# Performance work log

Measured on AMD Instinct MI355X. Metric: run time of the kernel, lower is better.

## Reference

```python
import jax, jax.numpy as jnp
import numpy as np

N = 50000       # nodes per batched graph
E = 800000      # edges per batched graph
G = 256         # graphs per batch (for max-node pooling)
VOCAB = 120     # node types == embedding vocab
D_EMB = 32
D_H = 100
D_FC = 32
MIN_TYPE = 5    # min_type_count in compute_node_pair_mmd
CAP = 25        # max_nodes_per_type (deterministic: first CAP nodes per type)
KER_MUL = 2.0   # standard multi-kernel Gaussian MMD settings
KER_NUM = 5


def setup_inputs() -> dict:
    key = jax.random.key(0)
    ks = jax.random.split(key, 16)
    ri = lambda k, sh, hi: jax.random.randint(k, sh, 0, hi, dtype=jnp.int32)
    feat = ri(ks[0], (N,), VOCAB)
    feat_src = ri(ks[1], (N,), VOCAB)
    feat_tar = ri(ks[2], (N,), VOCAB)
    edge_index = ri(ks[3], (2, E), N)
    edge_index_src = ri(ks[4], (2, E), N)
    edge_index_tar = ri(ks[5], (2, E), N)
    graph_ids = (jnp.arange(N, dtype=jnp.int32) * G) // N  # sorted, even partition
    mask = (jax.random.uniform(ks[6], (N,)) > 0.1).astype(jnp.float32)
    embed = jax.random.normal(ks[7], (VOCAB, D_EMB)) * 0.02
    gcn_w = jax.random.normal(ks[8], (D_EMB, D_H)) * (1.0 / np.sqrt(D_EMB))
    gcn_b = jnp.zeros((D_H,), jnp.float32)
    fc_w = jax.random.normal(ks[9], (D_H, D_FC)) * (1.0 / np.sqrt(D_H))
    fc_b = jnp.zeros((D_FC,), jnp.float32)
    def_w = jax.random.normal(ks[10], (D_FC, 1)) * (1.0 / np.sqrt(D_FC))
    def_b = jnp.zeros((1,), jnp.float32)
    return dict(feat=feat, feat_src=feat_src, feat_tar=feat_tar,
                edge_index=edge_index, edge_index_src=edge_index_src,
                edge_index_tar=edge_index_tar, graph_ids=graph_ids, mask=mask,
                embed=embed, gcn_w=gcn_w, gcn_b=gcn_b, fc_w=fc_w, fc_b=fc_b,
                def_w=def_w, def_b=def_b)


def _graph_conv(x, ei, w, b):
    # DGL GraphConv, norm='both': D_out^{-1/2} A^T D_in^{-1/2} X W + b (degrees clamped to 1)
    src, dst = ei[0], ei[1]
    ones = jnp.ones((ei.shape[1],), x.dtype)
    outdeg = jnp.clip(jax.ops.segment_sum(ones, src, num_segments=N), 1.0)
    indeg = jnp.clip(jax.ops.segment_sum(ones, dst, num_segments=N), 1.0)
    h = (x @ w) * (outdeg ** -0.5)[:, None]          # [N, D_H], weight first (in<=out)
    agg = jax.ops.segment_sum(h[src], dst, num_segments=N)
    return agg * (indeg ** -0.5)[:, None] + b


def _mmd(src_types, tgt_types, src_feats, tgt_feats):
    # per-type multi-kernel Gaussian MMD; deterministic cap of CAP nodes/type
    def per_type(t):
        sm = (src_types == t)
        tm = (tgt_types == t)
        s_cnt = sm.sum()
        t_cnt = tm.sum()
        sv, si = jax.lax.top_k(sm.astype(jnp.float32), CAP)  # first CAP indices of type t
        tv, ti = jax.lax.top_k(tm.astype(jnp.float32), CAP)
        X = jnp.concatenate([src_feats[si], tgt_feats[ti]], 0)      # [2C, D]
        valid = jnp.concatenate([sv, tv]) > 0                        # [2C]
        pm = valid[:, None] & valid[None, :]
        D2 = jnp.sum((X[:, None, :] - X[None, :, :]) ** 2, -1)      # [2C, 2C]
        m = jnp.minimum(s_cnt, CAP).astype(jnp.float32)
        n = jnp.minimum(t_cnt, CAP).astype(jnp.float32)
        ntot = m + n
        bw = jnp.sum(jnp.where(pm, D2, 0.0)) / jnp.maximum(ntot * ntot - ntot, 1.0)
        bw = bw / (KER_MUL ** (KER_NUM // 2))
        bws = bw * (KER_MUL ** jnp.arange(KER_NUM, dtype=jnp.float32))
        K = jnp.sum(jnp.exp(-D2[None] / jnp.maximum(bws, 1e-8)[:, None, None]), 0)
        K = jnp.where(pm, K, 0.0)
        XX = K[:CAP, :CAP].sum() / jnp.maximum(m * m, 1.0)
        YY = K[CAP:, CAP:].sum() / jnp.maximum(n * n, 1.0)
        XY = K[:CAP, CAP:].sum() / jnp.maximum(m * n, 1.0)
        loss = XX + YY - 2.0 * XY
        inc = (s_cnt >= MIN_TYPE) & (t_cnt >= MIN_TYPE)
        return jnp.where(inc, loss, 0.0), inc.astype(jnp.float32)
    losses, incs = jax.vmap(per_type)(jnp.arange(1, VOCAB, dtype=jnp.int32))  # type 0 skipped
    cnt = incs.sum()
    return jnp.where(cnt > 0, losses.sum() / jnp.maximum(cnt, 1.0), 0.0)


def reference(feat, feat_src, feat_tar, edge_index, edge_index_src, edge_index_tar,
              graph_ids, mask, embed, gcn_w, gcn_b, fc_w, fc_b, def_w, def_b):
    def process(f, ei, msk):
        x = embed[f]
        if msk is not None:
            x = x * msk[:, None]
        h = jax.nn.relu(_graph_conv(x, ei, gcn_w, gcn_b))            # node feats 'h'
        pooled = jax.ops.segment_max(h, graph_ids, num_segments=G,
                                     indices_are_sorted=True)        # dgl.max_nodes
        return h, pooled

    _, pool = process(feat, edge_index, mask)
    h_src, pool_src = process(feat_src, edge_index_src, None)
    h_tar, pool_tar = process(feat_tar, edge_index_tar, None)

    x_batch_mmd = pool @ fc_w + fc_b        # [G, 32]
    x_src_mmd = pool_src @ fc_w + fc_b
    x_tar_mmd = pool_tar @ fc_w + fc_b
    src_node_feat = h_src @ fc_w + fc_b     # [N, 32]
    tgt_node_feat = h_tar @ fc_w + fc_b
    x_loss_mmd_node = _mmd(feat_src, feat_tar, src_node_feat, tgt_node_feat)
    defect_prob = jax.nn.sigmoid(x_batch_mmd @ def_w + def_b)  # [G, 1]
    # domain_clf output is not returned by the original forward, so it is skipped here.
    return (x_batch_mmd, defect_prob, x_src_mmd, x_tar_mmd, x_loss_mmd_node)
```

## Files before the change

kernel.cpp:

```cpp
#include <hip/hip_runtime.h>
#include <hip/hip_bf16.h>

#define Nn 50000
#define Ee 800000
#define Gg 256
#define VOC 120
#define DH 100
#define CAPc 25
#define NTYPE 119
#define NCHUNK 196
#define DR 4
#define DS 32
#define DWORDS 6250
#define NBIN 391
#define EBLK 782

__global__ void t_kernel(const float* __restrict__ embed, const float* __restrict__ gcn_w,
                         float* __restrict__ Tp) {
    int t = blockIdx.x;
    int j = threadIdx.x;
    if (j < DH) {
        float acc = 0.f;
#pragma unroll
        for (int k = 0; k < 32; ++k) acc = fmaf(embed[t * 32 + k], gcn_w[k * DH + j], acc);
        Tp[t * DH + j] = acc;
    }
}

__global__ void selcount_kernel(const int* __restrict__ feat_src, const int* __restrict__ feat_tar,
                                int* __restrict__ chunkcnt) {
    int chunk = blockIdx.x, side = blockIdx.y;
    const int* f = side ? feat_tar : feat_src;
    __shared__ int hist[VOC];
    int tid = threadIdx.x;
    if (tid < VOC) hist[tid] = 0;
    __syncthreads();
    int i = chunk * 256 + tid;
    if (i < Nn) atomicAdd(&hist[f[i]], 1);
    __syncthreads();
    if (tid < VOC) chunkcnt[(side * NCHUNK + chunk) * VOC + tid] = hist[tid];
}

__global__ __launch_bounds__(64) void selprefix_kernel(const int* __restrict__ chunkcnt,
                                                       int* __restrict__ base,
                                                       int* __restrict__ fullcnt) {
    int pair = blockIdx.x;
    int side = pair / VOC, t = pair - side * VOC;
    int lane = threadIdx.x;
    int run = 0;
    for (int c0 = 0; c0 < NCHUNK; c0 += 64) {
        int c = c0 + lane;
        int v = (c < NCHUNK) ? chunkcnt[(side * NCHUNK + c) * VOC + t] : 0;
        int inc = v;
#pragma unroll
        for (int o = 1; o < 64; o <<= 1) {
            int u = __shfl_up(inc, o, 64);
            if (lane >= o) inc += u;
        }
        if (c < NCHUNK) base[(side * NCHUNK + c) * VOC + t] = run + inc - v;
        run += __shfl(inc, 63, 64);
    }
    if (lane == 0) fullcnt[side * VOC + t] = run;
}

__global__ void selgather_kernel(const int* __restrict__ feat_src, const int* __restrict__ feat_tar,
                                 const int* __restrict__ base, int* __restrict__ selpos_src,
                                 int* __restrict__ selpos_tar) {
    int chunk = blockIdx.x, side = blockIdx.y;
    const int* f = side ? feat_tar : feat_src;
    int* selpos = side ? selpos_tar : selpos_src;
    __shared__ int types[256];
    int tid = threadIdx.x;
    int i = chunk * 256 + tid;
    int t = (i < Nn) ? f[i] : -1;
    types[tid] = t;
    int bv = 0;
    bool need = (t >= 1);
    if (need) {
        bv = base[(side * NCHUNK + chunk) * VOC + t];
        need = (bv < CAPc);
    }
    int any = __syncthreads_count((int)need);
    if (any == 0) return;
    if (need) {
        int rank = bv;
        for (int q = 0; q < 256; ++q)
            if (q < tid && types[q] == t) rank++;
        if (rank < CAPc) selpos[i] = (t - 1) * CAPc + rank;
    }
}

__global__ __launch_bounds__(256) void deghist_kernel(
        const int* __restrict__ ei0, const int* __restrict__ ei1, const int* __restrict__ ei2,
        int* __restrict__ partial) {
    int g = blockIdx.y;
    int r = blockIdx.x & (DR - 1), s = blockIdx.x >> 2;
    const int* ei = (g == 0) ? ei0 : (g == 1) ? ei1 : ei2;
    const uint4* a4 = (const uint4*)(ei + s * (Ee / DS));
    __shared__ int hist[DWORDS];
    int tid = threadIdx.x;
    for (int i = tid; i < DWORDS; i += 256) hist[i] = 0;
    __syncthreads();
    unsigned base = r * (2 * DWORDS);
    for (int idx = tid; idx < (Ee / DS) / 4; idx += 256) {
        uint4 v = a4[idx];
        unsigned q;
        q = v.x - base; if (q < 2 * DWORDS) atomicAdd(&hist[q >> 1], 1 << ((q & 1) * 16));
        q = v.y - base; if (q < 2 * DWORDS) atomicAdd(&hist[q >> 1], 1 << ((q & 1) * 16));
        q = v.z - base; if (q < 2 * DWORDS) atomicAdd(&hist[q >> 1], 1 << ((q & 1) * 16));
        q = v.w - base; if (q < 2 * DWORDS) atomicAdd(&hist[q >> 1], 1 << ((q & 1) * 16));
    }
    __syncthreads();
    int* outp = partial + ((size_t)(g * DR + r) * DS + s) * DWORDS;
    for (int i = tid; i < DWORDS; i += 256) outp[i] = hist[i];
}

__global__ __launch_bounds__(256) void degmerge_kernel(
        const int* __restrict__ partial,
        const int* __restrict__ feat0, const int* __restrict__ feat1, const int* __restrict__ feat2,
        const float* __restrict__ mask, float2* __restrict__ pc) {
    int idx = blockIdx.x * 256 + threadIdx.x;
    if (idx >= 3 * DR * DWORDS) return;
    int g = idx / (DR * DWORDS);
    int rem = idx - g * (DR * DWORDS);
    int r = rem / DWORDS, w = rem - r * DWORDS;
    const int* p = partial + ((size_t)(g * DR + r) * DS) * DWORDS + w;
    int sum = 0;
#pragma unroll 8
    for (int s = 0; s < DS; ++s) sum += p[s * DWORDS];
    int c0 = sum & 0xFFFF, c1 = sum >> 16;
    int n0 = r * (2 * DWORDS) + 2 * w;
    const int* ft = (g == 0) ? feat0 : (g == 1) ? feat1 : feat2;
    float cf0 = rsqrtf((float)max(c0, 1));
    float cf1 = rsqrtf((float)max(c1, 1));
    if (g == 0) {
        cf0 *= mask[n0];
        cf1 *= mask[n0 + 1];
    }
    float4 v = make_float4(cf0, __int_as_float(ft[n0]), cf1, __int_as_float(ft[n0 + 1]));
    ((float4*)(pc + (size_t)g * Nn))[r * DWORDS + w] = v;
}

__global__ __launch_bounds__(256) void bincount_kernel(const int* __restrict__ ei0,
                                                       const int* __restrict__ ei1,
                                                       const int* __restrict__ ei2,
                                                       int* __restrict__ cntbuf) {
    int g = blockIdx.y;
    const int* dst = ((g == 0) ? ei0 : (g == 1) ? ei1 : ei2) + Ee;
    __shared__ int cnt[NBIN];
    int tid = threadIdx.x;
    for (int i = tid; i < NBIN; i += 256) cnt[i] = 0;
    __syncthreads();
    int e0 = (blockIdx.x * 256 + tid) * 4;
    if (e0 < Ee) {
        uint4 d = *(const uint4*)&dst[e0];
        atomicAdd(&cnt[d.x >> 7], 1);
        atomicAdd(&cnt[d.y >> 7], 1);
        atomicAdd(&cnt[d.z >> 7], 1);
        atomicAdd(&cnt[d.w >> 7], 1);
    }
    __syncthreads();
    for (int i = tid; i < NBIN; i += 256)
        cntbuf[((size_t)g * NBIN + i) * EBLK + blockIdx.x] = cnt[i];
}

__global__ __launch_bounds__(64) void binprefix_kernel(const int* __restrict__ cntbuf,
                                                       int* __restrict__ ofsbuf,
                                                       int* __restrict__ bintot) {
    int pair = blockIdx.x;
    const int* src = cntbuf + (size_t)pair * EBLK;
    int* dst = ofsbuf + (size_t)pair * EBLK;
    int lane = threadIdx.x;
    int run = 0;
    for (int c0 = 0; c0 < EBLK; c0 += 64) {
        int c = c0 + lane;
        int v = (c < EBLK) ? src[c] : 0;
        int inc = v;
#pragma unroll
        for (int o = 1; o < 64; o <<= 1) {
            int u = __shfl_up(inc, o, 64);
            if (lane >= o) inc += u;
        }
        if (c < EBLK) dst[c] = run + inc - v;
        run += __shfl(inc, 63, 64);
    }
    if (lane == 0) bintot[pair] = run;
}

__global__ __launch_bounds__(64) void binbase_kernel(const int* __restrict__ bintot,
                                                     int* __restrict__ binbase) {
    int g = blockIdx.x;
    int lane = threadIdx.x;
    int run = 0;
    for (int c0 = 0; c0 < NBIN; c0 += 64) {
        int c = c0 + lane;
        int v = (c < NBIN) ? bintot[g * NBIN + c] : 0;
        int inc = v;
#pragma unroll
        for (int o = 1; o < 64; o <<= 1) {
            int u = __shfl_up(inc, o, 64);
            if (lane >= o) inc += u;
        }
        if (c < NBIN) binbase[g * NBIN + c] = run + inc - v;
        run += __shfl(inc, 63, 64);
    }
}

__global__ __launch_bounds__(256) void binscatter_kernel(const int* __restrict__ ei0,
                                                         const int* __restrict__ ei1,
                                                         const int* __restrict__ ei2,
                                                         const int* __restrict__ ofsbuf,
                                                         const int* __restrict__ binbase,
                                                         unsigned* __restrict__ ebuf) {
    int g = blockIdx.y;
    const int* ei = (g == 0) ? ei0 : (g == 1) ? ei1 : ei2;
    __shared__ int cur[NBIN];
    int tid = threadIdx.x;
    for (int i = tid; i < NBIN; i += 256)
        cur[i] = binbase[g * NBIN + i] + ofsbuf[((size_t)g * NBIN + i) * EBLK + blockIdx.x];
    __syncthreads();
    unsigned* eb = ebuf + (size_t)g * Ee;
    int e0 = (blockIdx.x * 256 + tid) * 4;
    if (e0 < Ee) {
        uint4 s = *(const uint4*)&ei[e0];
        uint4 d = *(const uint4*)&ei[Ee + e0];
        int p;
        p = atomicAdd(&cur[d.x >> 7], 1); eb[p] = ((d.x & 127u) << 16) | s.x;
        p = atomicAdd(&cur[d.y >> 7], 1); eb[p] = ((d.y & 127u) << 16) | s.y;
        p = atomicAdd(&cur[d.z >> 7], 1); eb[p] = ((d.z & 127u) << 16) | s.z;
        p = atomicAdd(&cur[d.w >> 7], 1); eb[p] = ((d.w & 127u) << 16) | s.w;
    }
}

__global__ __launch_bounds__(256, 2) void fused_wh_kernel(const unsigned* __restrict__ ebuf,
                                                          const float2* __restrict__ pc,
                                                          const int* __restrict__ binbase,
                                                          const int* __restrict__ bintot,
                                                          const float* __restrict__ Tp,
                                                          const int* __restrict__ selposall,
                                                          float* __restrict__ h_sel,
                                                          const float* __restrict__ gcn_b,
                                                          float* __restrict__ pool) {
    __shared__ float Wl[VOC * 128];
    __shared__ int cnt[128];
    int g = blockIdx.y, bin = blockIdx.x;
    int tid = threadIdx.x;

    float4* Wl4 = (float4*)Wl;
#pragma unroll
    for (int i = 0; i < 15; ++i) Wl4[tid + i * 256] = make_float4(0.f, 0.f, 0.f, 0.f);
    if (tid < 128) cnt[tid] = 0;
    __syncthreads();

    int base = binbase[g * NBIN + bin];
    int n = bintot[g * NBIN + bin];
    const unsigned* eb = ebuf + (size_t)g * Ee + base;
    const float2* pcg = pc + (size_t)g * Nn;
    for (int i = tid; i < n; i += 256) {
        unsigned e = eb[i];
        float2 p = pcg[e & 0xFFFFu];
        int dl = e >> 16;
        atomicAdd(&Wl[__float_as_int(p.y) * 128 + dl], p.x);
        atomicAdd(&cnt[dl], 1);
    }
    __syncthreads();

    int lane = tid & 63, wv = tid >> 6;
    int chcol = __builtin_amdgcn_readfirstlane(wv) * 25;
    const float* Tc = Tp + chcol;
    int r0 = bin * 128;
    int nr = min(128, Nn - r0);
    float accA[25], accB[25];
#pragma unroll
    for (int j = 0; j < 25; ++j) { accA[j] = 0.f; accB[j] = 0.f; }

    for (int t0 = 0; t0 < VOC; t0 += 8) {
        float wA8[8], wB8[8];
#pragma unroll
        for (int u = 0; u < 8; ++u) {
            wA8[u] = Wl[(t0 + u) * 128 + lane];
            wB8[u] = Wl[(t0 + u) * 128 + lane + 64];
        }
#pragma unroll
        for (int u = 0; u < 8; ++u) {
            const float* tr = Tc + (t0 + u) * DH;
#pragma unroll
            for (int j = 0; j < 25; ++j) {
                float tv = tr[j];
                accA[j] = fmaf(wA8[u], tv, accA[j]);
                accB[j] = fmaf(wB8[u], tv, accB[j]);
            }
        }
    }

    int rA = lane, rB = lane + 64;
    bool vA = rA < nr, vB = rB < nr;
    float rsA = vA ? rsqrtf((float)max(cnt[rA], 1)) : 0.f;
    float rsB = vB ? rsqrtf((float)max(cnt[rB], 1)) : 0.f;
    int growA = r0 + rA, growB = r0 + rB;
    int seg0 = (r0 * Gg) / Nn;
    int segA = (growA * Gg) / Nn, segB = (growB * Gg) / Nn;
    float bb[25];
#pragma unroll
    for (int j = 0; j < 25; ++j) bb[j] = gcn_b[wv * 25 + j];

    float v0[25], v1[25];
#pragma unroll
    for (int j = 0; j < 25; ++j) {
        float hA = vA ? fmaxf(fmaf(accA[j], rsA, bb[j]), 0.f) : 0.f;
        float hB = vB ? fmaxf(fmaf(accB[j], rsB, bb[j]), 0.f) : 0.f;
        accA[j] = hA;
        accB[j] = hB;
        v0[j] = fmaxf((vA && segA == seg0) ? hA : 0.f, (vB && segB == seg0) ? hB : 0.f);
        v1[j] = fmaxf((vA && segA != seg0) ? hA : 0.f, (vB && segB != seg0) ? hB : 0.f);
    }
#pragma unroll
    for (int m = 1; m < 64; m <<= 1) {
#pragma unroll
        for (int j = 0; j < 25; ++j) {
            v0[j] = fmaxf(v0[j], __shfl_xor(v0[j], m, 64));
            v1[j] = fmaxf(v1[j], __shfl_xor(v1[j], m, 64));
        }
    }
    if (lane == 0) {
        float* poolg = pool + g * (Gg * DH) + seg0 * DH + wv * 25;
        for (int j = 0; j < 25; ++j) atomicMax((int*)&poolg[j], __float_as_int(v0[j]));
        int segLast = ((r0 + nr - 1) * Gg) / Nn;
        if (segLast != seg0)
            for (int j = 0; j < 25; ++j) atomicMax((int*)&poolg[DH + j], __float_as_int(v1[j]));
    }

    if (g > 0) {
        const int* selpos = selposall + (size_t)(g - 1) * Nn;
        float* hs = h_sel + (size_t)(g == 2 ? NTYPE * CAPc * DH : 0);
        int spA = vA ? selpos[growA] : -1;
        int spB = vB ? selpos[growB] : -1;
        if (spA >= 0) {
            float* d = hs + (size_t)spA * DH + wv * 25;
            for (int j = 0; j < 25; ++j) d[j] = accA[j];
        }
        if (spB >= 0) {
            float* d = hs + (size_t)spB * DH + wv * 25;
            for (int j = 0; j < 25; ++j) d[j] = accB[j];
        }
    }
}

__global__ void poolgemm_kernel(const float* __restrict__ pool, const float* __restrict__ fc_w,
                                const float* __restrict__ fc_b, const float* __restrict__ def_w,
                                const float* __restrict__ def_b, float* __restrict__ out) {
    int g = blockIdx.x;
    __shared__ float xb[32];
    int tid = threadIdx.x;
    if (tid < 96) {
        int p = tid >> 5, j = tid & 31;
        float acc = fc_b[j];
        const float* pr = pool + p * (Gg * DH) + g * DH;
#pragma unroll 4
        for (int k = 0; k < DH; ++k) acc = fmaf(pr[k], fc_w[k * 32 + j], acc);
        int off = (p == 0) ? 0 : (p == 1 ? 8448 : 16640);
        out[off + g * 32 + j] = acc;
        if (p == 0) xb[j] = acc;
    }
    __syncthreads();
    if (tid < 32) {
        float v = xb[tid] * def_w[tid];
        for (int o = 16; o; o >>= 1) v += __shfl_down(v, o, 64);
        if (tid == 0) out[8192 + g] = 1.f / (1.f + expf(-(v + def_b[0])));
    }
}

__global__ __launch_bounds__(256) void xfeat_kernel(const float* __restrict__ h_sel,
                                                    const int* __restrict__ fullcnt,
                                                    const float* __restrict__ fc_w,
                                                    const float* __restrict__ fc_b,
                                                    float* __restrict__ X) {
    int t = blockIdx.x;
    __shared__ float fw[DH * 32];
    for (int i = threadIdx.x; i < DH * 32; i += 256) fw[i] = fc_w[i];
    __syncthreads();
    int cs = min(fullcnt[t + 1], CAPc);
    int ct = min(fullcnt[VOC + t + 1], CAPc);
    int j = threadIdx.x & 31, rg = threadIdx.x >> 5;
    for (int r = rg; r < 2 * CAPc; r += 8) {
        int side = r / CAPc, rr = r % CAPc;
        int cnt = side ? ct : cs;
        float acc = 0.f;
        if (rr < cnt) {
            const float* hr = h_sel + ((size_t)side * NTYPE * CAPc + (size_t)t * CAPc + rr) * DH;
            acc = fc_b[j];
#pragma unroll 4
            for (int k = 0; k < DH; ++k) acc = fmaf(hr[k], fw[k * 32 + j], acc);
        }
        X[(size_t)t * 1600 + r * 32 + j] = acc;
    }
}

__device__ __forceinline__ float block_reduce256(float v, float* red, int tid) {
    __syncthreads();
    red[tid] = v;
    __syncthreads();
    for (int s = 128; s > 0; s >>= 1) {
        if (tid < s) red[tid] += red[tid + s];
        __syncthreads();
    }
    return red[0];
}

__global__ __launch_bounds__(256) void mmd_kernel(const float* __restrict__ X,
                                                  const int* __restrict__ fullcnt,
                                                  float* __restrict__ losses) {
    int t = blockIdx.x;
    __shared__ float Xs[50 * 32];
    __shared__ float D2[50 * 50];
    __shared__ float red[256];
    int tid = threadIdx.x;
    for (int i = tid; i < 1600; i += 256) Xs[i] = X[(size_t)t * 1600 + i];
    __syncthreads();
    int scF = fullcnt[t + 1];
    int tcF = fullcnt[VOC + t + 1];
    int m = min(scF, CAPc), n2 = min(tcF, CAPc);
    float bwpart = 0.f;
    for (int idx = tid; idx < 2500; idx += 256) {
        int i = idx / 50, j = idx % 50;
        float d = 0.f;
#pragma unroll
        for (int k = 0; k < 32; ++k) {
            float df = Xs[i * 32 + k] - Xs[j * 32 + k];
            d = fmaf(df, df, d);
        }
        D2[idx] = d;
        bool vi = (i < CAPc) ? (i < m) : (i - CAPc < n2);
        bool vj = (j < CAPc) ? (j < m) : (j - CAPc < n2);
        if (vi && vj) bwpart += d;
    }
    float bwsum = block_reduce256(bwpart, red, tid);
    float ntot = (float)(m + n2);
    float bw = bwsum / fmaxf(ntot * ntot - ntot, 1.f) * 0.25f;
    float bws[5];
#pragma unroll
    for (int k = 0; k < 5; ++k) bws[k] = fmaxf(bw * (float)(1 << k), 1e-8f);
    float xx = 0.f, yy = 0.f, xy = 0.f;
    for (int idx = tid; idx < 2500; idx += 256) {
        int i = idx / 50, j = idx % 50;
        bool vi = (i < CAPc) ? (i < m) : (i - CAPc < n2);
        bool vj = (j < CAPc) ? (j < m) : (j - CAPc < n2);
        if (!(vi && vj)) continue;
        float d = D2[idx];
        float kv = 0.f;
#pragma unroll
        for (int k = 0; k < 5; ++k) kv += expf(-d / bws[k]);
        if (i < CAPc && j < CAPc) xx += kv;
        else if (i >= CAPc && j >= CAPc) yy += kv;
        else if (i < CAPc) xy += kv;
    }
    float rxx = block_reduce256(xx, red, tid);
    float ryy = block_reduce256(yy, red, tid);
    float rxy = block_reduce256(xy, red, tid);
    if (tid == 0) {
        float fm = (float)m, fn = (float)n2;
        float XX = rxx / fmaxf(fm * fm, 1.f);
        float YY = ryy / fmaxf(fn * fn, 1.f);
        float XY = rxy / fmaxf(fm * fn, 1.f);
        float loss = XX + YY - 2.f * XY;
        int inc = (scF >= 5 && tcF >= 5) ? 1 : 0;
        losses[t * 2 + 0] = inc ? loss : 0.f;
        losses[t * 2 + 1] = (float)inc;
    }
}

__global__ void final_kernel(const float* __restrict__ losses, float* __restrict__ out) {
    __shared__ float red[128], redc[128];
    int tid = threadIdx.x;
    float s = 0.f, c = 0.f;
    for (int t = tid; t < NTYPE; t += 128) {
        s += losses[t * 2];
        c += losses[t * 2 + 1];
    }
    red[tid] = s;
    redc[tid] = c;
    __syncthreads();
    for (int st = 64; st > 0; st >>= 1) {
        if (tid < st) {
            red[tid] += red[tid + st];
            redc[tid] += redc[tid + st];
        }
        __syncthreads();
    }
    if (tid == 0) out[24832] = redc[0] > 0.f ? red[0] / fmaxf(redc[0], 1.f) : 0.f;
}

extern "C" void kernel_launch(void* const* d_in, const int* in_sizes, int n_in,
                              void* d_out, int out_size, void* d_ws, size_t ws_size,
                              hipStream_t stream) {
    const int* feat = (const int*)d_in[0];
    const int* feat_src = (const int*)d_in[1];
    const int* feat_tar = (const int*)d_in[2];
    const int* ei0 = (const int*)d_in[3];
    const int* ei1 = (const int*)d_in[4];
    const int* ei2 = (const int*)d_in[5];
    const float* mask = (const float*)d_in[7];
    const float* embed = (const float*)d_in[8];
    const float* gcn_w = (const float*)d_in[9];
    const float* gcn_b = (const float*)d_in[10];
    const float* fc_w = (const float*)d_in[11];
    const float* fc_b = (const float*)d_in[12];
    const float* def_w = (const float*)d_in[13];
    const float* def_b = (const float*)d_in[14];
    float* out = (float*)d_out;

    char* wsb = (char*)d_ws;
    int* partial = (int*)(wsb + 0);
    float* Tp = (float*)(wsb + 9600000);
    float* pool = (float*)(wsb + 9660000);
    float2* pc = (float2*)(wsb + 9967200);
    int* selpos = (int*)(wsb + 11167200);
    float* h_sel = (float*)(wsb + 11567200);
    int* fullcnt = (int*)(wsb + 13947200);
    float* X = (float*)(wsb + 13948160);
    float* losses = (float*)(wsb + 14709760);
    int* chunkcnt = (int*)(wsb + 14710720);
    int* baseb = (int*)(wsb + 14898880);
    int* cntbuf = (int*)(wsb + 15087040);
    int* ofsbuf = (int*)(wsb + 18756200);
    int* bintot = (int*)(wsb + 22425400);
    int* binbase = (int*)(wsb + 22430400);
    unsigned* ebuf = (unsigned*)(wsb + 22435200);

    hipMemsetAsync(pool, 0, 3 * Gg * DH * sizeof(float), stream);
    hipMemsetAsync(selpos, 0xFF, 2 * Nn * sizeof(int), stream);

    t_kernel<<<VOC, 128, 0, stream>>>(embed, gcn_w, Tp);

    selcount_kernel<<<dim3(NCHUNK, 2), 256, 0, stream>>>(feat_src, feat_tar, chunkcnt);
    selprefix_kernel<<<2 * VOC, 64, 0, stream>>>(chunkcnt, baseb, fullcnt);
    selgather_kernel<<<dim3(NCHUNK, 2), 256, 0, stream>>>(feat_src, feat_tar, baseb,
                                                          selpos, selpos + Nn);

    bincount_kernel<<<dim3(EBLK, 3), 256, 0, stream>>>(ei0, ei1, ei2, cntbuf);
    binprefix_kernel<<<3 * NBIN, 64, 0, stream>>>(cntbuf, ofsbuf, bintot);
    binbase_kernel<<<3, 64, 0, stream>>>(bintot, binbase);
    binscatter_kernel<<<dim3(EBLK, 3), 256, 0, stream>>>(ei0, ei1, ei2, ofsbuf, binbase, ebuf);

    deghist_kernel<<<dim3(DR * DS, 3), 256, 0, stream>>>(ei0, ei1, ei2, partial);
    degmerge_kernel<<<(3 * DR * DWORDS + 255) / 256, 256, 0, stream>>>(partial, feat, feat_src,
                                                                       feat_tar, mask, pc);

    fused_wh_kernel<<<dim3(NBIN, 3), 256, 0, stream>>>(ebuf, pc, binbase, bintot, Tp, selpos,
                                                       h_sel, gcn_b, pool);

    poolgemm_kernel<<<Gg, 128, 0, stream>>>(pool, fc_w, fc_b, def_w, def_b, out);
    xfeat_kernel<<<NTYPE, 256, 0, stream>>>(h_sel, fullcnt, fc_w, fc_b, X);
    mmd_kernel<<<NTYPE, 256, 0, stream>>>(X, fullcnt, losses);
    final_kernel<<<1, 128, 0, stream>>>(losses, out);
}
```

Measured before the change: 250.1 us.

## Split per-bin type-weight LDS accumulation into two type-range passes

New measurement: 296.4 us. +18.5%, slower.

```diff
diff --git a/kernel.cpp b/kernel.cpp
--- a/kernel.cpp
+++ b/kernel.cpp
@@ -14,6 +14,7 @@
 #define DWORDS 6250
 #define NBIN 391
 #define EBLK 782
+#define TCH2 60
 
 __global__ void t_kernel(const float* __restrict__ embed, const float* __restrict__ gcn_w,
                          float* __restrict__ Tp) {
@@ -241,58 +242,82 @@
                                                           float* __restrict__ h_sel,
                                                           const float* __restrict__ gcn_b,
                                                           float* __restrict__ pool) {
-    __shared__ float Wl[VOC * 128];
+    __shared__ float Wl[TCH2 * 128];
     __shared__ int cnt[128];
     int g = blockIdx.y, bin = blockIdx.x;
     int tid = threadIdx.x;
-
-    float4* Wl4 = (float4*)Wl;
-#pragma unroll
-    for (int i = 0; i < 15; ++i) Wl4[tid + i * 256] = make_float4(0.f, 0.f, 0.f, 0.f);
     if (tid < 128) cnt[tid] = 0;
-    __syncthreads();
 
     int base = binbase[g * NBIN + bin];
     int n = bintot[g * NBIN + bin];
     const unsigned* eb = ebuf + (size_t)g * Ee + base;
     const float2* pcg = pc + (size_t)g * Nn;
-    for (int i = tid; i < n; i += 256) {
-        unsigned e = eb[i];
-        float2 p = pcg[e & 0xFFFFu];
-        int dl = e >> 16;
-        atomicAdd(&Wl[__float_as_int(p.y) * 128 + dl], p.x);
-        atomicAdd(&cnt[dl], 1);
-    }
-    __syncthreads();
 
     int lane = tid & 63, wv = tid >> 6;
-    int chcol = __builtin_amdgcn_readfirstlane(wv) * 25;
-    const float* Tc = Tp + chcol;
+    const float* Tc = Tp + wv * 25;
+    float accA[25], accB[25];
+#pragma unroll
+    for (int j = 0; j < 25; ++j) { accA[j] = 0.f; accB[j] = 0.f; }
+
+    float4* Wl4 = (float4*)Wl;
+    for (int pass = 0; pass < 2; ++pass) {
+        __syncthreads();
+#pragma unroll
+        for (int i = 0; i < 8; ++i) {
+            int idx = tid + i * 256;
+            if (idx < TCH2 * 32) Wl4[idx] = make_float4(0.f, 0.f, 0.f, 0.f);
+        }
+        __syncthreads();
+        int tlo = pass * TCH2;
+        for (int i = tid; i < n; i += 256) {
+            unsigned e = eb[i];
+            float2 p = pcg[e & 0xFFFFu];
+            int dl = e >> 16;
+            if (pass == 0) atomicAdd(&cnt[dl], 1);
+            unsigned tq = (unsigned)(__float_as_int(p.y) - tlo);
+            if (tq < TCH2) atomicAdd(&Wl[tq * 128 + dl], p.x);
+        }
+        __syncthreads();
+        const float* Tb = Tc + tlo * DH;
+        for (int t0 = 0; t0 < TCH2; t0 += 4) {
+            float w0A = Wl[(t0 + 0) * 128 + lane];
+            float w0B = Wl[(t0 + 0) * 128 + lane + 64];
+            float w1A = Wl[(t0 + 1) * 128 + lane];
+            float w1B = Wl[(t0 + 1) * 128 + lane + 64];
+            float w2A = Wl[(t0 + 2) * 128 + lane];
+            float w2B = Wl[(t0 + 2) * 128 + lane + 64];
+            float w3A = Wl[(t0 + 3) * 128 + lane];
+            float w3B = Wl[(t0 + 3) * 128 + lane + 64];
+            const float* tr = Tb + t0 * DH;
+#pragma unroll
+            for (int j = 0; j < 25; ++j) {
+                float tv = tr[j];
+                accA[j] = fmaf(w0A, tv, accA[j]);
+                accB[j] = fmaf(w0B, tv, accB[j]);
+            }
+#pragma unroll
+            for (int j = 0; j < 25; ++j) {
+                float tv = tr[DH + j];
+                accA[j] = fmaf(w1A, tv, accA[j]);
+                accB[j] = fmaf(w1B, tv, accB[j]);
+            }
+#pragma unroll
+            for (int j = 0; j < 25; ++j) {
+                float tv = tr[2 * DH + j];
+                accA[j] = fmaf(w2A, tv, accA[j]);
+                accB[j] = fmaf(w2B, tv, accB[j]);
+            }
+#pragma unroll
+            for (int j = 0; j < 25; ++j) {
+                float tv = tr[3 * DH + j];
+                accA[j] = fmaf(w3A, tv, accA[j]);
+                accB[j] = fmaf(w3B, tv, accB[j]);
+            }
+        }
+    }
+
     int r0 = bin * 128;
     int nr = min(128, Nn - r0);
-    float accA[25], accB[25];
-#pragma unroll
-    for (int j = 0; j < 25; ++j) { accA[j] = 0.f; accB[j] = 0.f; }
-
-    for (int t0 = 0; t0 < VOC; t0 += 8) {
-        float wA8[8], wB8[8];
-#pragma unroll
-        for (int u = 0; u < 8; ++u) {
-            wA8[u] = Wl[(t0 + u) * 128 + lane];
-            wB8[u] = Wl[(t0 + u) * 128 + lane + 64];
-        }
-#pragma unroll
-        for (int u = 0; u < 8; ++u) {
-            const float* tr = Tc + (t0 + u) * DH;
-#pragma unroll
-            for (int j = 0; j < 25; ++j) {
-                float tv = tr[j];
-                accA[j] = fmaf(wA8[u], tv, accA[j]);
-                accB[j] = fmaf(wB8[u], tv, accB[j]);
-            }
-        }
-    }
-
     int rA = lane, rB = lane + 64;
     bool vA = rA < nr, vB = rB < nr;
     float rsA = vA ? rsqrtf((float)max(cnt[rA], 1)) : 0.f;
```

## Merge independent stage kernels into block-dispatched launches to cut launch count

Applied to the files above, without the earlier changes.

New measurement: 215.0 us. -14.0%, faster.

```diff
diff --git a/kernel.cpp b/kernel.cpp
--- a/kernel.cpp
+++ b/kernel.cpp
@@ -15,176 +15,147 @@
 #define NBIN 391
 #define EBLK 782
 
-__global__ void t_kernel(const float* __restrict__ embed, const float* __restrict__ gcn_w,
-                         float* __restrict__ Tp) {
-    int t = blockIdx.x;
-    int j = threadIdx.x;
-    if (j < DH) {
-        float acc = 0.f;
-#pragma unroll
-        for (int k = 0; k < 32; ++k) acc = fmaf(embed[t * 32 + k], gcn_w[k * DH + j], acc);
-        Tp[t * DH + j] = acc;
-    }
-}
-
-__global__ void selcount_kernel(const int* __restrict__ feat_src, const int* __restrict__ feat_tar,
-                                int* __restrict__ chunkcnt) {
-    int chunk = blockIdx.x, side = blockIdx.y;
-    const int* f = side ? feat_tar : feat_src;
-    __shared__ int hist[VOC];
+#define P1_T 0
+#define P1_SEL 120
+#define P1_BIN 512
+#define P1_DEG 2858
+#define P1_PCLR 3242
+#define P1_SCLR 3317
+#define P1_TOT 3415
+#define P3_SELG 0
+#define P3_BSC 392
+#define P3_DMG 2738
+#define P3_TOT 3031
+
+__global__ __launch_bounds__(256) void prep_kernel(
+        const float* __restrict__ embed, const float* __restrict__ gcn_w, float* __restrict__ Tp,
+        const int* __restrict__ feat_src, const int* __restrict__ feat_tar,
+        int* __restrict__ chunkcnt,
+        const int* __restrict__ ei0, const int* __restrict__ ei1, const int* __restrict__ ei2,
+        int* __restrict__ cntbuf, int* __restrict__ partial,
+        float* __restrict__ pool, int* __restrict__ selpos) {
+    __shared__ int sm[DWORDS];
+    int bx = blockIdx.x;
     int tid = threadIdx.x;
-    if (tid < VOC) hist[tid] = 0;
-    __syncthreads();
-    int i = chunk * 256 + tid;
-    if (i < Nn) atomicAdd(&hist[f[i]], 1);
-    __syncthreads();
-    if (tid < VOC) chunkcnt[(side * NCHUNK + chunk) * VOC + tid] = hist[tid];
-}
-
-__global__ __launch_bounds__(64) void selprefix_kernel(const int* __restrict__ chunkcnt,
-                                                       int* __restrict__ base,
-                                                       int* __restrict__ fullcnt) {
-    int pair = blockIdx.x;
-    int side = pair / VOC, t = pair - side * VOC;
+
+    if (bx < P1_SEL) {
+        int t = bx - P1_T;
+        if (tid < DH) {
+            float acc = 0.f;
+#pragma unroll
+            for (int k = 0; k < 32; ++k) acc = fmaf(embed[t * 32 + k], gcn_w[k * DH + tid], acc);
+            Tp[t * DH + tid] = acc;
+        }
+        return;
+    }
+    if (bx < P1_BIN) {
+        int idx = bx - P1_SEL;
+        int side = idx / NCHUNK, chunk = idx - side * NCHUNK;
+        const int* f = side ? feat_tar : feat_src;
+        if (tid < VOC) sm[tid] = 0;
+        __syncthreads();
+        int i = chunk * 256 + tid;
+        if (i < Nn) atomicAdd(&sm[f[i]], 1);
+        __syncthreads();
+        if (tid < VOC) chunkcnt[(side * NCHUNK + chunk) * VOC + tid] = sm[tid];
+        return;
+    }
+    if (bx < P1_DEG) {
+        int idx = bx - P1_BIN;
+        int g = idx / EBLK, blk = idx - g * EBLK;
+        const int* dst = ((g == 0) ? ei0 : (g == 1) ? ei1 : ei2) + Ee;
+        for (int i = tid; i < NBIN; i += 256) sm[i] = 0;
+        __syncthreads();
+        int e0 = (blk * 256 + tid) * 4;
+        if (e0 < Ee) {
+            uint4 d = *(const uint4*)&dst[e0];
+            atomicAdd(&sm[d.x >> 7], 1);
+            atomicAdd(&sm[d.y >> 7], 1);
+            atomicAdd(&sm[d.z >> 7], 1);
+            atomicAdd(&sm[d.w >> 7], 1);
+        }
+        __syncthreads();
+        for (int i = tid; i < NBIN; i += 256)
+            cntbuf[((size_t)g * NBIN + i) * EBLK + blk] = sm[i];
+        return;
+    }
+    if (bx < P1_PCLR) {
+        int idx = bx - P1_DEG;
+        int g = idx / (DR * DS), rs = idx - g * (DR * DS);
+        int r = rs & (DR - 1), s = rs >> 2;
+        const int* ei = (g == 0) ? ei0 : (g == 1) ? ei1 : ei2;
+        const uint4* a4 = (const uint4*)(ei + s * (Ee / DS));
+        for (int i = tid; i < DWORDS; i += 256) sm[i] = 0;
+        __syncthreads();
+        unsigned base = r * (2 * DWORDS);
+        for (int idx2 = tid; idx2 < (Ee / DS) / 4; idx2 += 256) {
+            uint4 v = a4[idx2];
+            unsigned q;
+            q = v.x - base; if (q < 2 * DWORDS) atomicAdd(&sm[q >> 1], 1 << ((q & 1) * 16));
+            q = v.y - base; if (q < 2 * DWORDS) atomicAdd(&sm[q >> 1], 1 << ((q & 1) * 16));
+            q = v.z - base; if (q < 2 * DWORDS) atomicAdd(&sm[q >> 1], 1 << ((q & 1) * 16));
+            q = v.w - base; if (q < 2 * DWORDS) atomicAdd(&sm[q >> 1], 1 << ((q & 1) * 16));
+        }
+        __syncthreads();
+        int* outp = partial + ((size_t)(g * DR + r) * DS + s) * DWORDS;
+        for (int i = tid; i < DWORDS; i += 256) outp[i] = sm[i];
+        return;
+    }
+    if (bx < P1_SCLR) {
+        int i = (bx - P1_PCLR) * 256 + tid;
+        ((float4*)pool)[i] = make_float4(0.f, 0.f, 0.f, 0.f);
+        return;
+    }
+    {
+        int i = (bx - P1_SCLR) * 256 + tid;
+        if (i < 25000) ((int4*)selpos)[i] = make_int4(-1, -1, -1, -1);
+        return;
+    }
+}
+
+__global__ __launch_bounds__(64) void prefix_kernel(const int* __restrict__ chunkcnt,
+                                                    int* __restrict__ baseb,
+                                                    int* __restrict__ fullcnt,
+                                                    const int* __restrict__ cntbuf,
+                                                    int* __restrict__ ofsbuf,
+                                                    int* __restrict__ bintot) {
+    int bx = blockIdx.x;
     int lane = threadIdx.x;
-    int run = 0;
-    for (int c0 = 0; c0 < NCHUNK; c0 += 64) {
-        int c = c0 + lane;
-        int v = (c < NCHUNK) ? chunkcnt[(side * NCHUNK + c) * VOC + t] : 0;
-        int inc = v;
-#pragma unroll
-        for (int o = 1; o < 64; o <<= 1) {
-            int u = __shfl_up(inc, o, 64);
-            if (lane >= o) inc += u;
-        }
-        if (c < NCHUNK) base[(side * NCHUNK + c) * VOC + t] = run + inc - v;
-        run += __shfl(inc, 63, 64);
-    }
-    if (lane == 0) fullcnt[side * VOC + t] = run;
-}
-
-__global__ void selgather_kernel(const int* __restrict__ feat_src, const int* __restrict__ feat_tar,
-                                 const int* __restrict__ base, int* __restrict__ selpos_src,
-                                 int* __restrict__ selpos_tar) {
-    int chunk = blockIdx.x, side = blockIdx.y;
-    const int* f = side ? feat_tar : feat_src;
-    int* selpos = side ? selpos_tar : selpos_src;
-    __shared__ int types[256];
-    int tid = threadIdx.x;
-    int i = chunk * 256 + tid;
-    int t = (i < Nn) ? f[i] : -1;
-    types[tid] = t;
-    int bv = 0;
-    bool need = (t >= 1);
-    if (need) {
-        bv = base[(side * NCHUNK + chunk) * VOC + t];
-        need = (bv < CAPc);
-    }
-    int any = __syncthreads_count((int)need);
-    if (any == 0) return;
-    if (need) {
-        int rank = bv;
-        for (int q = 0; q < 256; ++q)
-            if (q < tid && types[q] == t) rank++;
-        if (rank < CAPc) selpos[i] = (t - 1) * CAPc + rank;
-    }
-}
-
-__global__ __launch_bounds__(256) void deghist_kernel(
-        const int* __restrict__ ei0, const int* __restrict__ ei1, const int* __restrict__ ei2,
-        int* __restrict__ partial) {
-    int g = blockIdx.y;
-    int r = blockIdx.x & (DR - 1), s = blockIdx.x >> 2;
-    const int* ei = (g == 0) ? ei0 : (g == 1) ? ei1 : ei2;
-    const uint4* a4 = (const uint4*)(ei + s * (Ee / DS));
-    __shared__ int hist[DWORDS];
-    int tid = threadIdx.x;
-    for (int i = tid; i < DWORDS; i += 256) hist[i] = 0;
-    __syncthreads();
-    unsigned base = r * (2 * DWORDS);
-    for (int idx = tid; idx < (Ee / DS) / 4; idx += 256) {
-        uint4 v = a4[idx];
-        unsigned q;
-        q = v.x - base; if (q < 2 * DWORDS) atomicAdd(&hist[q >> 1], 1 << ((q & 1) * 16));
-        q = v.y - base; if (q < 2 * DWORDS) atomicAdd(&hist[q >> 1], 1 << ((q & 1) * 16));
-        q = v.z - base; if (q < 2 * DWORDS) atomicAdd(&hist[q >> 1], 1 << ((q & 1) * 16));
-        q = v.w - base; if (q < 2 * DWORDS) atomicAdd(&hist[q >> 1], 1 << ((q & 1) * 16));
-    }
-    __syncthreads();
-    int* outp = partial + ((size_t)(g * DR + r) * DS + s) * DWORDS;
-    for (int i = tid; i < DWORDS; i += 256) outp[i] = hist[i];
-}
-
-__global__ __launch_bounds__(256) void degmerge_kernel(
-        const int* __restrict__ partial,
-        const int* __restrict__ feat0, const int* __restrict__ feat1, const int* __restrict__ feat2,
-        const float* __restrict__ mask, float2* __restrict__ pc) {
-    int idx = blockIdx.x * 256 + threadIdx.x;
-    if (idx >= 3 * DR * DWORDS) return;
-    int g = idx / (DR * DWORDS);
-    int rem = idx - g * (DR * DWORDS);
-    int r = rem / DWORDS, w = rem - r * DWORDS;
-    const int* p = partial + ((size_t)(g * DR + r) * DS) * DWORDS + w;
-    int sum = 0;
-#pragma unroll 8
-    for (int s = 0; s < DS; ++s) sum += p[s * DWORDS];
-    int c0 = sum & 0xFFFF, c1 = sum >> 16;
-    int n0 = r * (2 * DWORDS) + 2 * w;
-    const int* ft = (g == 0) ? feat0 : (g == 1) ? feat1 : feat2;
-    float cf0 = rsqrtf((float)max(c0, 1));
-    float cf1 = rsqrtf((float)max(c1, 1));
-    if (g == 0) {
-        cf0 *= mask[n0];
-        cf1 *= mask[n0 + 1];
-    }
-    float4 v = make_float4(cf0, __int_as_float(ft[n0]), cf1, __int_as_float(ft[n0 + 1]));
-    ((float4*)(pc + (size_t)g * Nn))[r * DWORDS + w] = v;
-}
-
-__global__ __launch_bounds__(256) void bincount_kernel(const int* __restrict__ ei0,
-                                                       const int* __restrict__ ei1,
-                                                       const int* __restrict__ ei2,
-                                                       int* __restrict__ cntbuf) {
-    int g = blockIdx.y;
-    const int* dst = ((g == 0) ? ei0 : (g == 1) ? ei1 : ei2) + Ee;
-    __shared__ int cnt[NBIN];
-    int tid = threadIdx.x;
-    for (int i = tid; i < NBIN; i += 256) cnt[i] = 0;
-    __syncthreads();
-    int e0 = (blockIdx.x * 256 + tid) * 4;
-    if (e0 < Ee) {
-        uint4 d = *(const uint4*)&dst[e0];
-        atomicAdd(&cnt[d.x >> 7], 1);
-        atomicAdd(&cnt[d.y >> 7], 1);
-        atomicAdd(&cnt[d.z >> 7], 1);
-        atomicAdd(&cnt[d.w >> 7], 1);
-    }
-    __syncthreads();
-    for (int i = tid; i < NBIN; i += 256)
-        cntbuf[((size_t)g * NBIN + i) * EBLK + blockIdx.x] = cnt[i];
-}
-
-__global__ __launch_bounds__(64) void binprefix_kernel(const int* __restrict__ cntbuf,
-                                                       int* __restrict__ ofsbuf,
-                                                       int* __restrict__ bintot) {
-    int pair = blockIdx.x;
-    const int* src = cntbuf + (size_t)pair * EBLK;
-    int* dst = ofsbuf + (size_t)pair * EBLK;
-    int lane = threadIdx.x;
-    int run = 0;
-    for (int c0 = 0; c0 < EBLK; c0 += 64) {
-        int c = c0 + lane;
-        int v = (c < EBLK) ? src[c] : 0;
-        int inc = v;
-#pragma unroll
-        for (int o = 1; o < 64; o <<= 1) {
-            int u = __shfl_up(inc, o, 64);
-            if (lane >= o) inc += u;
-        }
-        if (c < EBLK) dst[c] = run + inc - v;
-        run += __shfl(inc, 63, 64);
-    }
-    if (lane == 0) bintot[pair] = run;
+    if (bx < 2 * VOC) {
+        int side = bx / VOC, t = bx - side * VOC;
+        int run = 0;
+        for (int c0 = 0; c0 < NCHUNK; c0 += 64) {
+            int c = c0 + lane;
+            int v = (c < NCHUNK) ? chunkcnt[(side * NCHUNK + c) * VOC + t] : 0;
+            int inc = v;
+#pragma unroll
+            for (int o = 1; o < 64; o <<= 1) {
+                int u = __shfl_up(inc, o, 64);
+                if (lane >= o) inc += u;
+            }
+            if (c < NCHUNK) baseb[(side * NCHUNK + c) * VOC + t] = run + inc - v;
+            run += __shfl(inc, 63, 64);
+        }
+        if (lane == 0) fullcnt[side * VOC + t] = run;
+    } else {
+        int pair = bx - 2 * VOC;
+        const int* src = cntbuf + (size_t)pair * EBLK;
+        int* dst = ofsbuf + (size_t)pair * EBLK;
+        int run = 0;
+        for (int c0 = 0; c0 < EBLK; c0 += 64) {
+            int c = c0 + lane;
+            int v = (c < EBLK) ? src[c] : 0;
+            int inc = v;
+#pragma unroll
+            for (int o = 1; o < 64; o <<= 1) {
+                int u = __shfl_up(inc, o, 64);
+                if (lane >= o) inc += u;
+            }
+            if (c < EBLK) dst[c] = run + inc - v;
+            run += __shfl(inc, 63, 64);
+        }
+        if (lane == 0) bintot[pair] = run;
+    }
 }
 
 __global__ __launch_bounds__(64) void binbase_kernel(const int* __restrict__ bintot,
@@ -206,29 +177,84 @@
     }
 }
 
-__global__ __launch_bounds__(256) void binscatter_kernel(const int* __restrict__ ei0,
-                                                         const int* __restrict__ ei1,
-                                                         const int* __restrict__ ei2,
-                                                         const int* __restrict__ ofsbuf,
-                                                         const int* __restrict__ binbase,
-                                                         unsigned* __restrict__ ebuf) {
-    int g = blockIdx.y;
-    const int* ei = (g == 0) ? ei0 : (g == 1) ? ei1 : ei2;
-    __shared__ int cur[NBIN];
+__global__ __launch_bounds__(256) void scatter_kernel(
+        const int* __restrict__ feat_src, const int* __restrict__ feat_tar,
+        const int* __restrict__ baseb, int* __restrict__ selpos_src, int* __restrict__ selpos_tar,
+        const int* __restrict__ ei0, const int* __restrict__ ei1, const int* __restrict__ ei2,
+        const int* __restrict__ ofsbuf, const int* __restrict__ binbase,
+        unsigned* __restrict__ ebuf,
+        const int* __restrict__ partial, const int* __restrict__ feat0,
+        const float* __restrict__ mask, float2* __restrict__ pc) {
+    __shared__ int sm[NBIN];
+    int bx = blockIdx.x;
     int tid = threadIdx.x;
-    for (int i = tid; i < NBIN; i += 256)
-        cur[i] = binbase[g * NBIN + i] + ofsbuf[((size_t)g * NBIN + i) * EBLK + blockIdx.x];
-    __syncthreads();
-    unsigned* eb = ebuf + (size_t)g * Ee;
-    int e0 = (blockIdx.x * 256 + tid) * 4;
-    if (e0 < Ee) {
-        uint4 s = *(const uint4*)&ei[e0];
-        uint4 d = *(const uint4*)&ei[Ee + e0];
-        int p;
-        p = atomicAdd(&cur[d.x >> 7], 1); eb[p] = ((d.x & 127u) << 16) | s.x;
-        p = atomicAdd(&cur[d.y >> 7], 1); eb[p] = ((d.y & 127u) << 16) | s.y;
-        p = atomicAdd(&cur[d.z >> 7], 1); eb[p] = ((d.z & 127u) << 16) | s.z;
-        p = atomicAdd(&cur[d.w >> 7], 1); eb[p] = ((d.w & 127u) << 16) | s.w;
+
+    if (bx < P3_BSC) {
+        int idx = bx - P3_SELG;
+        int side = idx / NCHUNK, chunk = idx - side * NCHUNK;
+        const int* f = side ? feat_tar : feat_src;
+        int* selpos = side ? selpos_tar : selpos_src;
+        int i = chunk * 256 + tid;
+        int t = (i < Nn) ? f[i] : -1;
+        sm[tid] = t;
+        int bv = 0;
+        bool need = (t >= 1);
+        if (need) {
+            bv = baseb[(side * NCHUNK + chunk) * VOC + t];
+            need = (bv < CAPc);
+        }
+        int any = __syncthreads_count((int)need);
+        if (any == 0) return;
+        if (need) {
+            int rank = bv;
+            for (int q = 0; q < 256; ++q)
+                if (q < tid && sm[q] == t) rank++;
+            if (rank < CAPc) selpos[i] = (t - 1) * CAPc + rank;
+        }
+        return;
+    }
+    if (bx < P3_DMG) {
+        int idx = bx - P3_BSC;
+        int g = idx / EBLK, blk = idx - g * EBLK;
+        const int* ei = (g == 0) ? ei0 : (g == 1) ? ei1 : ei2;
+        for (int i = tid; i < NBIN; i += 256)
+            sm[i] = binbase[g * NBIN + i] + ofsbuf[((size_t)g * NBIN + i) * EBLK + blk];
+        __syncthreads();
+        unsigned* eb = ebuf + (size_t)g * Ee;
+        int e0 = (blk * 256 + tid) * 4;
+        if (e0 < Ee) {
+            uint4 s = *(const uint4*)&ei[e0];
+            uint4 d = *(const uint4*)&ei[Ee + e0];
+            int p;
+            p = atomicAdd(&sm[d.x >> 7], 1); eb[p] = ((d.x & 127u) << 16) | s.x;
+            p = atomicAdd(&sm[d.y >> 7], 1); eb[p] = ((d.y & 127u) << 16) | s.y;
+            p = atomicAdd(&sm[d.z >> 7], 1); eb[p] = ((d.z & 127u) << 16) | s.z;
+            p = atomicAdd(&sm[d.w >> 7], 1); eb[p] = ((d.w & 127u) << 16) | s.w;
+        }
+        return;
+    }
+    {
+        int idx = (bx - P3_DMG) * 256 + tid;
+        if (idx >= 3 * DR * DWORDS) return;
+        int g = idx / (DR * DWORDS);
+        int rem = idx - g * (DR * DWORDS);
+        int r = rem / DWORDS, w = rem - r * DWORDS;
+        const int* p = partial + ((size_t)(g * DR + r) * DS) * DWORDS + w;
+        int sum = 0;
+#pragma unroll 8
+        for (int s = 0; s < DS; ++s) sum += p[s * DWORDS];
+        int c0 = sum & 0xFFFF, c1 = sum >> 16;
+        int n0 = r * (2 * DWORDS) + 2 * w;
+        const int* ft = (g == 0) ? feat0 : (g == 1) ? feat_src : feat_tar;
+        float cf0 = rsqrtf((float)max(c0, 1));
+        float cf1 = rsqrtf((float)max(c1, 1));
+        if (g == 0) {
+            cf0 *= mask[n0];
+            cf1 *= mask[n0 + 1];
+        }
+        float4 v = make_float4(cf0, __int_as_float(ft[n0]), cf1, __int_as_float(ft[n0 + 1]));
+        ((float4*)(pc + (size_t)g * Nn))[r * DWORDS + w] = v;
+        return;
     }
 }
 
@@ -346,53 +372,58 @@
     }
 }
 
-__global__ void poolgemm_kernel(const float* __restrict__ pool, const float* __restrict__ fc_w,
-                                const float* __restrict__ fc_b, const float* __restrict__ def_w,
-                                const float* __restrict__ def_b, float* __restrict__ out) {
-    int g = blockIdx.x;
-    __shared__ float xb[32];
+__global__ __launch_bounds__(256) void post_kernel(const float* __restrict__ pool,
+                                                   const float* __restrict__ fc_w,
+                                                   const float* __restrict__ fc_b,
+                                                   const float* __restrict__ def_w,
+                                                   const float* __restrict__ def_b,
+                                                   float* __restrict__ out,
+                                                   const float* __restrict__ h_sel,
+                                                   const int* __restrict__ fullcnt,
+                                                   float* __restrict__ X) {
+    __shared__ float smf[DH * 32];
+    int bx = blockIdx.x;
     int tid = threadIdx.x;
-    if (tid < 96) {
-        int p = tid >> 5, j = tid & 31;
-        float acc = fc_b[j];
-        const float* pr = pool + p * (Gg * DH) + g * DH;
+    if (bx < Gg) {
+        int g = bx;
+        if (tid < 96) {
+            int p = tid >> 5, j = tid & 31;
+            float acc = fc_b[j];
+            const float* pr = pool + p * (Gg * DH) + g * DH;
 #pragma unroll 4
-        for (int k = 0; k < DH; ++k) acc = fmaf(pr[k], fc_w[k * 32 + j], acc);
-        int off = (p == 0) ? 0 : (p == 1 ? 8448 : 16640);
-        out[off + g * 32 + j] = acc;
-        if (p == 0) xb[j] = acc;
-    }
-    __syncthreads();
-    if (tid < 32) {
-        float v = xb[tid] * def_w[tid];
-        for (int o = 16; o; o >>= 1) v += __shfl_down(v, o, 64);
-        if (tid == 0) out[8192 + g] = 1.f / (1.f + expf(-(v + def_b[0])));
-    }
-}
-
-__global__ __launch_bounds__(256) void xfeat_kernel(const float* __restrict__ h_sel,
-                                                    const int* __restrict__ fullcnt,
-                                                    const float* __restrict__ fc_w,
-                                                    const float* __restrict__ fc_b,
-                                                    float* __restrict__ X) {
-    int t = blockIdx.x;
-    __shared__ float fw[DH * 32];
-    for (int i = threadIdx.x; i < DH * 32; i += 256) fw[i] = fc_w[i];
-    __syncthreads();
-    int cs = min(fullcnt[t + 1], CAPc);
-    int ct = min(fullcnt[VOC + t + 1], CAPc);
-    int j = threadIdx.x & 31, rg = threadIdx.x >> 5;
-    for (int r = rg; r < 2 * CAPc; r += 8) {
-        int side = r / CAPc, rr = r % CAPc;
-        int cnt = side ? ct : cs;
-        float acc = 0.f;
-        if (rr < cnt) {
-            const float* hr = h_sel + ((size_t)side * NTYPE * CAPc + (size_t)t * CAPc + rr) * DH;
-            acc = fc_b[j];
+            for (int k = 0; k < DH; ++k) acc = fmaf(pr[k], fc_w[k * 32 + j], acc);
+            int off = (p == 0) ? 0 : (p == 1 ? 8448 : 16640);
+            out[off + g * 32 + j] = acc;
+            if (p == 0) smf[j] = acc;
+        }
+        __syncthreads();
+        if (tid < 32) {
+            float v = smf[tid] * def_w[tid];
+            for (int o = 16; o; o >>= 1) v += __shfl_down(v, o, 64);
+            if (tid == 0) out[8192 + g] = 1.f / (1.f + expf(-(v + def_b[0])));
+        }
+        return;
+    }
+    {
+        int t = bx - Gg;
+        for (int i = tid; i < DH * 32; i += 256) smf[i] = fc_w[i];
+        __syncthreads();
+        int cs = min(fullcnt[t + 1], CAPc);
+        int ct = min(fullcnt[VOC + t + 1], CAPc);
+        int j = tid & 31, rg = tid >> 5;
+        for (int r = rg; r < 2 * CAPc; r += 8) {
+            int side = r / CAPc, rr = r % CAPc;
+            int cnt = side ? ct : cs;
+            float acc = 0.f;
+            if (rr < cnt) {
+                const float* hr = h_sel + ((size_t)side * NTYPE * CAPc + (size_t)t * CAPc + rr) * DH;
+                acc = fc_b[j];
 #pragma unroll 4
-            for (int k = 0; k < DH; ++k) acc = fmaf(hr[k], fw[k * 32 + j], acc);
-        }
-        X[(size_t)t * 1600 + r * 32 + j] = acc;
+                for (int k = 0; k < DH; ++k) acc = fmaf(hr[k], smf[k * 32 + j], acc);
+            }
+            X[(size_t)t * 1600 + r * 32 + j] = acc;
+        }
+        return;
     }
 }
 
@@ -527,30 +558,18 @@
     int* binbase = (int*)(wsb + 22430400);
     unsigned* ebuf = (unsigned*)(wsb + 22435200);
 
-    hipMemsetAsync(pool, 0, 3 * Gg * DH * sizeof(float), stream);
-    hipMemsetAsync(selpos, 0xFF, 2 * Nn * sizeof(int), stream);
-
-    t_kernel<<<VOC, 128, 0, stream>>>(embed, gcn_w, Tp);
-
-    selcount_kernel<<<dim3(NCHUNK, 2), 256, 0, stream>>>(feat_src, feat_tar, chunkcnt);
-    selprefix_kernel<<<2 * VOC, 64, 0, stream>>>(chunkcnt, baseb, fullcnt);
-    selgather_kernel<<<dim3(NCHUNK, 2), 256, 0, stream>>>(feat_src, feat_tar, baseb,
-                                                          selpos, selpos + Nn);
-
-    bincount_kernel<<<dim3(EBLK, 3), 256, 0, stream>>>(ei0, ei1, ei2, cntbuf);
-    binprefix_kernel<<<3 * NBIN, 64, 0, stream>>>(cntbuf, ofsbuf, bintot);
+    prep_kernel<<<P1_TOT, 256, 0, stream>>>(embed, gcn_w, Tp, feat_src, feat_tar, chunkcnt,
+                                            ei0, ei1, ei2, cntbuf, partial, pool, selpos);
+    prefix_kernel<<<2 * VOC + 3 * NBIN, 64, 0, stream>>>(chunkcnt, baseb, fullcnt, cntbuf,
+                                                         ofsbuf, bintot);
     binbase_kernel<<<3, 64, 0, stream>>>(bintot, binbase);
-    binscatter_kernel<<<dim3(EBLK, 3), 256, 0, stream>>>(ei0, ei1, ei2, ofsbuf, binbase, ebuf);
-
-    deghist_kernel<<<dim3(DR * DS, 3), 256, 0, stream>>>(ei0, ei1, ei2, partial);
-    degmerge_kernel<<<(3 * DR * DWORDS + 255) / 256, 256, 0, stream>>>(partial, feat, feat_src,
-                                                                       feat_tar, mask, pc);
-
+    scatter_kernel<<<P3_TOT, 256, 0, stream>>>(feat_src, feat_tar, baseb, selpos, selpos + Nn,
+                                               ei0, ei1, ei2, ofsbuf, binbase, ebuf, partial,
+                                               feat, mask, pc);
     fused_wh_kernel<<<dim3(NBIN, 3), 256, 0, stream>>>(ebuf, pc, binbase, bintot, Tp, selpos,
                                                        h_sel, gcn_b, pool);
-
-    poolgemm_kernel<<<Gg, 128, 0, stream>>>(pool, fc_w, fc_b, def_w, def_b, out);
-    xfeat_kernel<<<NTYPE, 256, 0, stream>>>(h_sel, fullcnt, fc_w, fc_b, X);
+    post_kernel<<<Gg + NTYPE, 256, 0, stream>>>(pool, fc_w, fc_b, def_w, def_b, out, h_sel,
+                                                fullcnt, X);
     mmd_kernel<<<NTYPE, 256, 0, stream>>>(X, fullcnt, losses);
     final_kernel<<<1, 128, 0, stream>>>(losses, out);
 }
```
